# Kernel tuning notes

Measured on AMD Instinct MI355X. Metric: run time of the kernel, lower is better.

## Reference

```python
import jax, jax.numpy as jnp
import numpy as np

B, S, H, T = 32, 1024, 1024, 256
WINDOW = 2
ITERATIONS = 3


def setup_inputs() -> dict:
    key = jax.random.key(0)
    k1, k2, k3, k4, k5, k6 = jax.random.split(key, 6)
    token_feats = jax.random.normal(k1, (B, S, H), dtype=jnp.float32)
    unary_score = jax.random.normal(k2, (B, S, T), dtype=jnp.float32)
    lengths = jax.random.randint(k3, (B,), S // 2, S + 1)  # in [S/2, S]
    mask = (jnp.arange(S)[None, :] < lengths[:, None]).astype(jnp.float32)
    transitions = jax.random.normal(k4, (WINDOW, T, T), dtype=jnp.float32)
    start_transitions = jax.random.normal(k5, (WINDOW, T), dtype=jnp.float32)
    end_transitions = jax.random.normal(k6, (WINDOW, T), dtype=jnp.float32)
    return {
        "token_feats": token_feats,
        "unary_score": unary_score,
        "mask": mask,
        "transitions": transitions,
        "start_transitions": start_transitions,
        "end_transitions": end_transitions,
        "lengths": lengths,
    }


def reference(token_feats, unary_score, mask, transitions, start_transitions,
              end_transitions, lengths):
    # mask unary (and token_feats, as in original; token_feats is unused in
    # the plain-transitions second-order path)
    unary = unary_score * mask[..., None]        # [B,S,T]
    _ = token_feats * mask[..., None]
    q = unary
    batch_range = jnp.arange(q.shape[0])
    for _it in range(ITERATIONS):
        q = jax.nn.softmax(q, axis=-1)
        left_sum = jnp.zeros_like(q)
        right_sum = jnp.zeros_like(q)
        for j in range(1, WINDOW + 1):
            # message from left neighbor at distance j
            left_sum = left_sum.at[:, j:].add(
                jnp.einsum('nsa,ab->nsb', q[:, :-j], transitions[j - 1]))
            # message from right neighbor at distance j
            right_sum = right_sum.at[:, :-j].add(
                jnp.einsum('nsb,ab->nsa', q[:, j:], transitions[j - 1]))
            # end transitions scatter-add at position lengths - j
            right_sum = right_sum.at[batch_range, lengths - j].add(
                end_transitions[j - 1])
        msg = left_sum + right_sum
        # start transitions on first WINDOW positions (broadcast over batch)
        msg = msg.at[:, 0:WINDOW].add(start_transitions)
        q = unary + msg
        q = q * mask[..., None]
    return q
```

## Files before the change

### kernel.cpp

```cpp
#include <hip/hip_runtime.h>
#include <hip/hip_bf16.h>
#include <cstdint>


typedef __attribute__((ext_vector_type(4))) float f32x4;
typedef __attribute__((ext_vector_type(8))) short bf16x8;

__device__ __forceinline__ void load_lds16(const void* g, void* l) {
    __builtin_amdgcn_global_load_lds(
        (const __attribute__((address_space(1))) void*)g,
        (__attribute__((address_space(3))) void*)l, 16, 0, 0);
}

__global__ __launch_bounds__(256) void prep_wct(
    const float* __restrict__ trans,
    __hip_bfloat16* __restrict__ Pa, __hip_bfloat16* __restrict__ Pb,
    __hip_bfloat16* __restrict__ WcTt)
{
    int idx = blockIdx.x * 256 + threadIdx.x;
    if (idx < 32768) {
        int p = idx >> 10, sl = idx & 1023;
        int n = sl >> 2, cs = sl & 3;
        int gk = p * 4 + (cs ^ ((n >> 1) & 3));
        union { bf16x8 v; __hip_bfloat16 h[8]; } o;
        #pragma unroll
        for (int e = 0; e < 8; ++e) {
            int k = gk * 8 + e;
            int r = k >> 8, kk = k & 255;
            float v;
            if (r == 0)      v = trans[kk * 256 + n];
            else if (r == 1) v = trans[65536 + kk * 256 + n];
            else if (r == 2) v = trans[n * 256 + kk];
            else             v = trans[65536 + n * 256 + kk];
            o.h[e] = __float2bfloat16(v);
        }
        ((bf16x8*)WcTt)[idx] = o.v;
    } else if (idx < 40960) {
        int g = idx - 32768;
        __hip_bfloat16* P = (g & 4096) ? Pb : Pa;
        int rem = g & 4095;
        int b = rem >> 7, wr = (rem >> 5) & 3, ch = rem & 31;
        int row = b * 1028 + ((wr < 2) ? wr : 1024 + wr);
        bf16x8 z = {};
        *(bf16x8*)(P + row * 256 + ch * 8) = z;
    }
}

__global__ __launch_bounds__(512, 4) void mfvi_iter_k(
    const __hip_bfloat16* __restrict__ Pin,
    const __hip_bfloat16* __restrict__ WcTt,
    const float* __restrict__ unary, const int* __restrict__ lengths,
    const float* __restrict__ startT, const float* __restrict__ endT,
    __hip_bfloat16* __restrict__ Pout, float* __restrict__ out,
    int first_it, int final_it)
{
    __shared__ __hip_bfloat16 Ps[68 * 256];
    __shared__ __hip_bfloat16 Bs[2 * 256 * 32];
    __shared__ float redA[256];
    __shared__ float redB[256];

    int tid = threadIdx.x;
    int lane = tid & 63, w = tid >> 6;
    int cn = lane & 15, quad = lane >> 4;
    int wm = (w >> 2) * 32, wn = (w & 3) * 64;
    int nslice = w & 3;
    int tile = blockIdx.x;
    int b = tile >> 4, s0 = (tile & 15) << 6;
    int len = lengths[b];

    if (first_it) {
        for (int q = 0; q < 9; ++q) {
            int r = w + q * 8;
            if (r >= 68) break;
            int s = s0 + r - 2;
            int ch = lane >> 1;
            int slot = (ch & ~7) | ((ch ^ r) & 7);
            char* dst = (char*)Ps + r * 512 + slot * 16 + (lane & 1) * 8;
            if (s >= 0 && s < 1024) {
                float mval = (s < len) ? 1.f : 0.f;
                float4 x = *((const float4*)(unary + ((size_t)((b << 10) + s)) * 256 + lane * 4));
                x.x *= mval; x.y *= mval; x.z *= mval; x.w *= mval;
                float mx = fmaxf(fmaxf(x.x, x.y), fmaxf(x.z, x.w));
                #pragma unroll
                for (int o = 32; o; o >>= 1) mx = fmaxf(mx, __shfl_xor(mx, o));
                float ea = __expf(x.x - mx), eb = __expf(x.y - mx);
                float ec = __expf(x.z - mx), ed = __expf(x.w - mx);
                float sum = ea + eb + ec + ed;
                #pragma unroll
                for (int o = 32; o; o >>= 1) sum += __shfl_xor(sum, o);
                float inv = 1.0f / sum;
                union { ushort4 u; __hip_bfloat16 h[4]; } o4;
                o4.h[0] = __float2bfloat16(ea * inv);
                o4.h[1] = __float2bfloat16(eb * inv);
                o4.h[2] = __float2bfloat16(ec * inv);
                o4.h[3] = __float2bfloat16(ed * inv);
                *((ushort4*)dst) = o4.u;
            } else {
                ushort4 z = {0, 0, 0, 0};
                *((ushort4*)dst) = z;
            }
        }
    } else {
        const char* Pbase = (const char*)(Pin + ((size_t)b * 1028 + s0) * 256);
        #pragma unroll
        for (int t = 0; t < 5; ++t) {
            int c = t * 512 + tid;
            if (t < 4 || tid < 128) {
                int row = c >> 5, ch = c & 31;
                int gch = (ch & ~7) | ((ch ^ row) & 7);
                load_lds16(Pbase + row * 512 + gch * 16, (char*)Ps + c * 16);
            }
        }
    }
    __syncthreads();

    auto stageB = [&](int bb, int p) {
        #pragma unroll
        for (int c = 0; c < 2; ++c) {
            int sl = c * 512 + tid;
            load_lds16((const char*)WcTt + p * 16384 + sl * 16,
                       (char*)Bs + bb * 16384 + sl * 16);
        }
    };

    stageB(0, 0);
    stageB(1, 1);

    f32x4 acc[2][4] = {};

#define K_STEP(P, VMC, DOSTAGE) do {                                         \
    asm volatile("s_waitcnt vmcnt(" #VMC ")" ::: "memory");                  \
    __builtin_amdgcn_s_barrier();                                            \
    int region = (P) >> 3;                                                   \
    int delta = (region == 0) ? -1 : (region == 1) ? -2                      \
              : (region == 2) ?  1 : 2;                                      \
    int gcb = ((P) & 7) * 4 + quad;                                          \
    bf16x8 af[2], bfv[4];                                                    \
    _Pragma("unroll")                                                        \
    for (int i = 0; i < 2; ++i) {                                            \
        int r = wm + (i << 4) + cn + delta + 2;                              \
        int slot = (gcb & ~7) | ((gcb ^ r) & 7);                             \
        af[i] = *(const bf16x8*)((const char*)Ps + r * 512 + slot * 16);     \
    }                                                                        \
    _Pragma("unroll")                                                        \
    for (int j = 0; j < 4; ++j) {                                            \
        int n = wn + (j << 4) + cn;                                          \
        int cs = quad ^ ((n >> 1) & 3);                                      \
        bfv[j] = *(const bf16x8*)((const char*)Bs + ((P) & 1) * 16384        \
                                  + n * 64 + cs * 16);                       \
    }                                                                        \
    asm volatile("s_waitcnt lgkmcnt(0)" ::: "memory");                       \
    __builtin_amdgcn_s_barrier();                                            \
    if (DOSTAGE) stageB(((P) & 1), (P) + 2);                                 \
    __builtin_amdgcn_s_setprio(1);                                           \
    _Pragma("unroll")                                                        \
    for (int i = 0; i < 2; ++i)                                              \
        _Pragma("unroll")                                                    \
        for (int j = 0; j < 4; ++j)                                          \
            acc[i][j] = __builtin_amdgcn_mfma_f32_16x16x32_bf16(             \
                af[i], bfv[j], acc[i][j], 0, 0, 0);                          \
    __builtin_amdgcn_s_setprio(0);                                           \
} while (0)

    #pragma unroll
    for (int p = 0; p < 30; ++p) K_STEP(p, 2, true);
    K_STEP(30, 2, false);
    K_STEP(31, 0, false);
#undef K_STEP

    #pragma unroll
    for (int i = 0; i < 2; ++i)
        #pragma unroll
        for (int j = 0; j < 4; ++j) {
            int n = wn + (j << 4) + cn;
            #pragma unroll
            for (int r = 0; r < 4; ++r) {
                int s = s0 + wm + (i << 4) + (quad << 2) + r;
                float x = acc[i][j][r];
                if (s == 0)       x += startT[n];
                if (s == 1)       x += startT[256 + n];
                if (s == len - 1) x += endT[n];
                if (s == len - 2) x += endT[256 + n];
                long idx = ((long)((b << 10) + s)) * 256 + n;
                x += unary[idx];
                acc[i][j][r] = (s < len) ? x : 0.f;
            }
        }

    if (final_it) {
        #pragma unroll
        for (int i = 0; i < 2; ++i)
            #pragma unroll
            for (int j = 0; j < 4; ++j) {
                int n = wn + (j << 4) + cn;
                #pragma unroll
                for (int r = 0; r < 4; ++r) {
                    int s = s0 + wm + (i << 4) + (quad << 2) + r;
                    out[((long)((b << 10) + s)) * 256 + n] = acc[i][j][r];
                }
            }
        return;
    }

    #pragma unroll
    for (int i = 0; i < 2; ++i)
        #pragma unroll
        for (int r = 0; r < 4; ++r) {
            float m4 = fmaxf(fmaxf(acc[i][0][r], acc[i][1][r]),
                             fmaxf(acc[i][2][r], acc[i][3][r]));
            m4 = fmaxf(m4, __shfl_xor(m4, 1));
            m4 = fmaxf(m4, __shfl_xor(m4, 2));
            m4 = fmaxf(m4, __shfl_xor(m4, 4));
            m4 = fmaxf(m4, __shfl_xor(m4, 8));
            if (cn == 0)
                redA[(nslice << 6) + wm + (i << 4) + (quad << 2) + r] = m4;
        }
    __syncthreads();
    float M[2][4];
    #pragma unroll
    for (int i = 0; i < 2; ++i)
        #pragma unroll
        for (int r = 0; r < 4; ++r) {
            int row = wm + (i << 4) + (quad << 2) + r;
            M[i][r] = fmaxf(fmaxf(redA[row], redA[64 + row]),
                            fmaxf(redA[128 + row], redA[192 + row]));
        }
    #pragma unroll
    for (int i = 0; i < 2; ++i)
        #pragma unroll
        for (int r = 0; r < 4; ++r) {
            float s4 = 0.f;
            #pragma unroll
            for (int j = 0; j < 4; ++j) {
                float e = __expf(acc[i][j][r] - M[i][r]);
                acc[i][j][r] = e;
                s4 += e;
            }
            s4 += __shfl_xor(s4, 1);
            s4 += __shfl_xor(s4, 2);
            s4 += __shfl_xor(s4, 4);
            s4 += __shfl_xor(s4, 8);
            if (cn == 0)
                redB[(nslice << 6) + wm + (i << 4) + (quad << 2) + r] = s4;
        }
    __syncthreads();
    #pragma unroll
    for (int i = 0; i < 2; ++i)
        #pragma unroll
        for (int r = 0; r < 4; ++r) {
            int row = wm + (i << 4) + (quad << 2) + r;
            float inv = 1.0f / (redB[row] + redB[64 + row] +
                                redB[128 + row] + redB[192 + row]);
            int s = s0 + row;
            #pragma unroll
            for (int j = 0; j < 4; ++j) {
                int n = wn + (j << 4) + cn;
                Pout[((size_t)b * 1028 + 2 + s) * 256 + n] =
                    __float2bfloat16(acc[i][j][r] * inv);
            }
        }
}

extern "C" void kernel_launch(void* const* d_in, const int* in_sizes, int n_in,
                              void* d_out, int out_size, void* d_ws, size_t ws_size,
                              hipStream_t stream) {
    const float* unary  = (const float*)d_in[1];
    const float* trans  = (const float*)d_in[3];
    const float* startT = (const float*)d_in[4];
    const float* endT   = (const float*)d_in[5];
    const int*   lens   = (const int*)d_in[6];

    char* ws = (char*)d_ws;
    __hip_bfloat16* Pa   = (__hip_bfloat16*)ws;
    __hip_bfloat16* Pb   = (__hip_bfloat16*)(ws + ((size_t)32 << 20));
    __hip_bfloat16* WcTt = (__hip_bfloat16*)(ws + ((size_t)64 << 20));
    float* out = (float*)d_out;

    prep_wct<<<dim3(160), dim3(256), 0, stream>>>(trans, Pa, Pb, WcTt);
    mfvi_iter_k<<<dim3(512), dim3(512), 0, stream>>>(Pa, WcTt, unary, lens, startT, endT, Pb, nullptr, 1, 0);
    mfvi_iter_k<<<dim3(512), dim3(512), 0, stream>>>(Pb, WcTt, unary, lens, startT, endT, Pa, nullptr, 0, 0);
    mfvi_iter_k<<<dim3(512), dim3(512), 0, stream>>>(Pa, WcTt, unary, lens, startT, endT, nullptr, out, 0, 1);
}
```

Baseline: 278.7 us.

## Fuse three MFVI iterations into one kernel with halo recomputation

Replaces the three per-iteration launches with a single kernel that keeps q in LDS across all iterations. Each 64-row tile loads an 84-row window so the neighbor messages can be recomputed locally, using redundant halo rows instead of global round-trips. This removes the intermediate bf16 P buffers, two launches and the global write/read of q between iterations. In exchange each block does extra MFMA work for the 16 halo rows, with four of the eight waves carrying a third row tile, which unbalances the waves and adds LDS and register use.

Result: slower. 618.9 us (+122.1%).

```diff
diff --git a/kernel.cpp b/kernel.cpp
--- a/kernel.cpp
+++ b/kernel.cpp
@@ -13,106 +13,79 @@
 }
 
 __global__ __launch_bounds__(256) void prep_wct(
-    const float* __restrict__ trans,
-    __hip_bfloat16* __restrict__ Pa, __hip_bfloat16* __restrict__ Pb,
-    __hip_bfloat16* __restrict__ WcTt)
+    const float* __restrict__ trans, __hip_bfloat16* __restrict__ WcTt)
 {
     int idx = blockIdx.x * 256 + threadIdx.x;
-    if (idx < 32768) {
-        int p = idx >> 10, sl = idx & 1023;
-        int n = sl >> 2, cs = sl & 3;
-        int gk = p * 4 + (cs ^ ((n >> 1) & 3));
-        union { bf16x8 v; __hip_bfloat16 h[8]; } o;
-        #pragma unroll
-        for (int e = 0; e < 8; ++e) {
-            int k = gk * 8 + e;
-            int r = k >> 8, kk = k & 255;
-            float v;
-            if (r == 0)      v = trans[kk * 256 + n];
-            else if (r == 1) v = trans[65536 + kk * 256 + n];
-            else if (r == 2) v = trans[n * 256 + kk];
-            else             v = trans[65536 + n * 256 + kk];
-            o.h[e] = __float2bfloat16(v);
-        }
-        ((bf16x8*)WcTt)[idx] = o.v;
-    } else if (idx < 40960) {
-        int g = idx - 32768;
-        __hip_bfloat16* P = (g & 4096) ? Pb : Pa;
-        int rem = g & 4095;
-        int b = rem >> 7, wr = (rem >> 5) & 3, ch = rem & 31;
-        int row = b * 1028 + ((wr < 2) ? wr : 1024 + wr);
-        bf16x8 z = {};
-        *(bf16x8*)(P + row * 256 + ch * 8) = z;
+    int p = idx >> 10, sl = idx & 1023;
+    int n = sl >> 2, cs = sl & 3;
+    int gk = p * 4 + (cs ^ ((n >> 1) & 3));
+    union { bf16x8 v; __hip_bfloat16 h[8]; } o;
+    #pragma unroll
+    for (int e = 0; e < 8; ++e) {
+        int k = gk * 8 + e;
+        int r = k >> 8, kk = k & 255;
+        float v;
+        if (r == 0)      v = trans[kk * 256 + n];
+        else if (r == 1) v = trans[65536 + kk * 256 + n];
+        else if (r == 2) v = trans[n * 256 + kk];
+        else             v = trans[65536 + n * 256 + kk];
+        o.h[e] = __float2bfloat16(v);
     }
-}
-
-__global__ __launch_bounds__(512, 4) void mfvi_iter_k(
-    const __hip_bfloat16* __restrict__ Pin,
+    ((bf16x8*)WcTt)[idx] = o.v;
+}
+
+__global__ __launch_bounds__(512, 4) void mfvi_fused3(
     const __hip_bfloat16* __restrict__ WcTt,
     const float* __restrict__ unary, const int* __restrict__ lengths,
     const float* __restrict__ startT, const float* __restrict__ endT,
-    __hip_bfloat16* __restrict__ Pout, float* __restrict__ out,
-    int first_it, int final_it)
+    float* __restrict__ out)
 {
-    __shared__ __hip_bfloat16 Ps[68 * 256];
+    __shared__ __hip_bfloat16 Ps[84 * 256];
     __shared__ __hip_bfloat16 Bs[2 * 256 * 32];
-    __shared__ float redA[256];
-    __shared__ float redB[256];
+    __shared__ float redA[320];
+    __shared__ float redB[320];
 
     int tid = threadIdx.x;
     int lane = tid & 63, w = tid >> 6;
     int cn = lane & 15, quad = lane >> 4;
-    int wm = (w >> 2) * 32, wn = (w & 3) * 64;
+    bool wlo = (w < 4);
+    int wm = wlo ? 0 : 48, wn = (w & 3) * 64;
     int nslice = w & 3;
     int tile = blockIdx.x;
     int b = tile >> 4, s0 = (tile & 15) << 6;
     int len = lengths[b];
 
-    if (first_it) {
-        for (int q = 0; q < 9; ++q) {
-            int r = w + q * 8;
-            if (r >= 68) break;
-            int s = s0 + r - 2;
-            int ch = lane >> 1;
-            int slot = (ch & ~7) | ((ch ^ r) & 7);
-            char* dst = (char*)Ps + r * 512 + slot * 16 + (lane & 1) * 8;
-            if (s >= 0 && s < 1024) {
-                float mval = (s < len) ? 1.f : 0.f;
-                float4 x = *((const float4*)(unary + ((size_t)((b << 10) + s)) * 256 + lane * 4));
-                x.x *= mval; x.y *= mval; x.z *= mval; x.w *= mval;
-                float mx = fmaxf(fmaxf(x.x, x.y), fmaxf(x.z, x.w));
-                #pragma unroll
-                for (int o = 32; o; o >>= 1) mx = fmaxf(mx, __shfl_xor(mx, o));
-                float ea = __expf(x.x - mx), eb = __expf(x.y - mx);
-                float ec = __expf(x.z - mx), ed = __expf(x.w - mx);
-                float sum = ea + eb + ec + ed;
-                #pragma unroll
-                for (int o = 32; o; o >>= 1) sum += __shfl_xor(sum, o);
-                float inv = 1.0f / sum;
-                union { ushort4 u; __hip_bfloat16 h[4]; } o4;
-                o4.h[0] = __float2bfloat16(ea * inv);
-                o4.h[1] = __float2bfloat16(eb * inv);
-                o4.h[2] = __float2bfloat16(ec * inv);
-                o4.h[3] = __float2bfloat16(ed * inv);
-                *((ushort4*)dst) = o4.u;
-            } else {
-                ushort4 z = {0, 0, 0, 0};
-                *((ushort4*)dst) = z;
-            }
-        }
-    } else {
-        const char* Pbase = (const char*)(Pin + ((size_t)b * 1028 + s0) * 256);
-        #pragma unroll
-        for (int t = 0; t < 5; ++t) {
-            int c = t * 512 + tid;
-            if (t < 4 || tid < 128) {
-                int row = c >> 5, ch = c & 31;
-                int gch = (ch & ~7) | ((ch ^ row) & 7);
-                load_lds16(Pbase + row * 512 + gch * 16, (char*)Ps + c * 16);
-            }
+    for (int q = 0; q < 11; ++q) {
+        int pr = w + q * 8;
+        if (pr >= 84) break;
+        int s = s0 + pr - 10;
+        int ch = lane >> 1;
+        int slot = (ch & ~7) | ((ch ^ pr) & 7);
+        char* dst = (char*)Ps + pr * 512 + slot * 16 + (lane & 1) * 8;
+        if (s >= 0 && s < 1024) {
+            float mval = (s < len) ? 1.f : 0.f;
+            float4 x = *((const float4*)(unary + ((size_t)((b << 10) + s)) * 256 + lane * 4));
+            x.x *= mval; x.y *= mval; x.z *= mval; x.w *= mval;
+            float mx = fmaxf(fmaxf(x.x, x.y), fmaxf(x.z, x.w));
+            #pragma unroll
+            for (int o = 32; o; o >>= 1) mx = fmaxf(mx, __shfl_xor(mx, o));
+            float ea = __expf(x.x - mx), eb = __expf(x.y - mx);
+            float ec = __expf(x.z - mx), ed = __expf(x.w - mx);
+            float sum = ea + eb + ec + ed;
+            #pragma unroll
+            for (int o = 32; o; o >>= 1) sum += __shfl_xor(sum, o);
+            float inv = 1.0f / sum;
+            union { ushort4 u; __hip_bfloat16 h[4]; } o4;
+            o4.h[0] = __float2bfloat16(ea * inv);
+            o4.h[1] = __float2bfloat16(eb * inv);
+            o4.h[2] = __float2bfloat16(ec * inv);
+            o4.h[3] = __float2bfloat16(ed * inv);
+            *((ushort4*)dst) = o4.u;
+        } else {
+            ushort4 z = {0, 0, 0, 0};
+            *((ushort4*)dst) = z;
         }
     }
-    __syncthreads();
 
     auto stageB = [&](int bb, int p) {
         #pragma unroll
@@ -123,10 +96,13 @@
         }
     };
 
-    stageB(0, 0);
-    stageB(1, 1);
-
-    f32x4 acc[2][4] = {};
+    #pragma unroll 1
+    for (int it = 0; it < 3; ++it) {
+        __syncthreads();
+        stageB(0, 0);
+        stageB(1, 1);
+
+        f32x4 acc[3][4] = {};
 
 #define K_STEP(P, VMC, DOSTAGE) do {                                         \
     asm volatile("s_waitcnt vmcnt(" #VMC ")" ::: "memory");                  \
@@ -135,12 +111,17 @@
     int delta = (region == 0) ? -1 : (region == 1) ? -2                      \
               : (region == 2) ?  1 : 2;                                      \
     int gcb = ((P) & 7) * 4 + quad;                                          \
-    bf16x8 af[2], bfv[4];                                                    \
+    bf16x8 af[3], bfv[4];                                                    \
     _Pragma("unroll")                                                        \
     for (int i = 0; i < 2; ++i) {                                            \
         int r = wm + (i << 4) + cn + delta + 2;                              \
         int slot = (gcb & ~7) | ((gcb ^ r) & 7);                             \
         af[i] = *(const bf16x8*)((const char*)Ps + r * 512 + slot * 16);     \
+    }                                                                        \
+    if (wlo) {                                                               \
+        int r = 32 + cn + delta + 2;                                         \
+        int slot = (gcb & ~7) | ((gcb ^ r) & 7);                             \
+        af[2] = *(const bf16x8*)((const char*)Ps + r * 512 + slot * 16);     \
     }                                                                        \
     _Pragma("unroll")                                                        \
     for (int j = 0; j < 4; ++j) {                                            \
@@ -159,106 +140,132 @@
         for (int j = 0; j < 4; ++j)                                          \
             acc[i][j] = __builtin_amdgcn_mfma_f32_16x16x32_bf16(             \
                 af[i], bfv[j], acc[i][j], 0, 0, 0);                          \
+    if (wlo) {                                                               \
+        _Pragma("unroll")                                                    \
+        for (int j = 0; j < 4; ++j)                                          \
+            acc[2][j] = __builtin_amdgcn_mfma_f32_16x16x32_bf16(             \
+                af[2], bfv[j], acc[2][j], 0, 0, 0);                          \
+    }                                                                        \
     __builtin_amdgcn_s_setprio(0);                                           \
 } while (0)
 
-    #pragma unroll
-    for (int p = 0; p < 30; ++p) K_STEP(p, 2, true);
-    K_STEP(30, 2, false);
-    K_STEP(31, 0, false);
+        #pragma unroll
+        for (int p = 0; p < 30; ++p) K_STEP(p, 2, true);
+        K_STEP(30, 2, false);
+        K_STEP(31, 0, false);
 #undef K_STEP
 
-    #pragma unroll
-    for (int i = 0; i < 2; ++i)
-        #pragma unroll
-        for (int j = 0; j < 4; ++j) {
-            int n = wn + (j << 4) + cn;
-            #pragma unroll
-            for (int r = 0; r < 4; ++r) {
-                int s = s0 + wm + (i << 4) + (quad << 2) + r;
-                float x = acc[i][j][r];
-                if (s == 0)       x += startT[n];
-                if (s == 1)       x += startT[256 + n];
-                if (s == len - 1) x += endT[n];
-                if (s == len - 2) x += endT[256 + n];
-                long idx = ((long)((b << 10) + s)) * 256 + n;
-                x += unary[idx];
-                acc[i][j][r] = (s < len) ? x : 0.f;
-            }
-        }
-
-    if (final_it) {
-        #pragma unroll
-        for (int i = 0; i < 2; ++i)
+        #pragma unroll
+        for (int i = 0; i < 3; ++i) {
+            if (i == 2 && !wlo) continue;
             #pragma unroll
             for (int j = 0; j < 4; ++j) {
                 int n = wn + (j << 4) + cn;
                 #pragma unroll
                 for (int r = 0; r < 4; ++r) {
-                    int s = s0 + wm + (i << 4) + (quad << 2) + r;
-                    out[((long)((b << 10) + s)) * 256 + n] = acc[i][j][r];
-                }
-            }
-        return;
+                    int lr = wm + (i << 4) + (quad << 2) + r;
+                    int s = s0 + lr - 8;
+                    float x = acc[i][j][r];
+                    if (s == 0)       x += startT[n];
+                    if (s == 1)       x += startT[256 + n];
+                    if (s == len - 1) x += endT[n];
+                    if (s == len - 2) x += endT[256 + n];
+                    if (s >= 0 && s < 1024)
+                        x += unary[((long)((b << 10) + s)) * 256 + n];
+                    acc[i][j][r] = (s >= 0 && s < len) ? x : 0.f;
+                }
+            }
+        }
+
+        if (it == 2) {
+            #pragma unroll
+            for (int i = 0; i < 3; ++i) {
+                if (i == 2 && !wlo) continue;
+                #pragma unroll
+                for (int j = 0; j < 4; ++j) {
+                    int n = wn + (j << 4) + cn;
+                    #pragma unroll
+                    for (int r = 0; r < 4; ++r) {
+                        int lr = wm + (i << 4) + (quad << 2) + r;
+                        if (lr < 8 || lr >= 72) continue;
+                        int s = s0 + lr - 8;
+                        out[((long)((b << 10) + s)) * 256 + n] = acc[i][j][r];
+                    }
+                }
+            }
+            return;
+        }
+
+        #pragma unroll
+        for (int i = 0; i < 3; ++i) {
+            if (i == 2 && !wlo) continue;
+            #pragma unroll
+            for (int r = 0; r < 4; ++r) {
+                float m4 = fmaxf(fmaxf(acc[i][0][r], acc[i][1][r]),
+                                 fmaxf(acc[i][2][r], acc[i][3][r]));
+                m4 = fmaxf(m4, __shfl_xor(m4, 1));
+                m4 = fmaxf(m4, __shfl_xor(m4, 2));
+                m4 = fmaxf(m4, __shfl_xor(m4, 4));
+                m4 = fmaxf(m4, __shfl_xor(m4, 8));
+                if (cn == 0)
+                    redA[nslice * 80 + wm + (i << 4) + (quad << 2) + r] = m4;
+            }
+        }
+        __syncthreads();
+        float M[3][4];
+        #pragma unroll
+        for (int i = 0; i < 3; ++i) {
+            if (i == 2 && !wlo) continue;
+            #pragma unroll
+            for (int r = 0; r < 4; ++r) {
+                int lr = wm + (i << 4) + (quad << 2) + r;
+                M[i][r] = fmaxf(fmaxf(redA[lr], redA[80 + lr]),
+                                fmaxf(redA[160 + lr], redA[240 + lr]));
+            }
+        }
+        #pragma unroll
+        for (int i = 0; i < 3; ++i) {
+            if (i == 2 && !wlo) continue;
+            #pragma unroll
+            for (int r = 0; r < 4; ++r) {
+                float s4 = 0.f;
+                #pragma unroll
+                for (int j = 0; j < 4; ++j) {
+                    float e = __expf(acc[i][j][r] - M[i][r]);
+                    acc[i][j][r] = e;
+                    s4 += e;
+                }
+                s4 += __shfl_xor(s4, 1);
+                s4 += __shfl_xor(s4, 2);
+                s4 += __shfl_xor(s4, 4);
+                s4 += __shfl_xor(s4, 8);
+                if (cn == 0)
+                    redB[nslice * 80 + wm + (i << 4) + (quad << 2) + r] = s4;
+            }
+        }
+        __syncthreads();
+        #pragma unroll
+        for (int i = 0; i < 3; ++i) {
+            if (i == 2 && !wlo) continue;
+            #pragma unroll
+            for (int r = 0; r < 4; ++r) {
+                int lr = wm + (i << 4) + (quad << 2) + r;
+                int s = s0 + lr - 8;
+                bool inr = (s >= 0 && s < 1024);
+                float inv = 1.0f / (redB[lr] + redB[80 + lr] +
+                                    redB[160 + lr] + redB[240 + lr]);
+                int pr = lr + 2;
+                #pragma unroll
+                for (int j = 0; j < 4; ++j) {
+                    int n = wn + (j << 4) + cn;
+                    int ch = n >> 3;
+                    int slot = (ch & ~7) | ((ch ^ pr) & 7);
+                    *((__hip_bfloat16*)((char*)Ps + pr * 512 + slot * 16 + (n & 7) * 2)) =
+                        __float2bfloat16(inr ? acc[i][j][r] * inv : 0.f);
+                }
+            }
+        }
     }
-
-    #pragma unroll
-    for (int i = 0; i < 2; ++i)
-        #pragma unroll
-        for (int r = 0; r < 4; ++r) {
-            float m4 = fmaxf(fmaxf(acc[i][0][r], acc[i][1][r]),
-                             fmaxf(acc[i][2][r], acc[i][3][r]));
-            m4 = fmaxf(m4, __shfl_xor(m4, 1));
-            m4 = fmaxf(m4, __shfl_xor(m4, 2));
-            m4 = fmaxf(m4, __shfl_xor(m4, 4));
-            m4 = fmaxf(m4, __shfl_xor(m4, 8));
-            if (cn == 0)
-                redA[(nslice << 6) + wm + (i << 4) + (quad << 2) + r] = m4;
-        }
-    __syncthreads();
-    float M[2][4];
-    #pragma unroll
-    for (int i = 0; i < 2; ++i)
-        #pragma unroll
-        for (int r = 0; r < 4; ++r) {
-            int row = wm + (i << 4) + (quad << 2) + r;
-            M[i][r] = fmaxf(fmaxf(redA[row], redA[64 + row]),
-                            fmaxf(redA[128 + row], redA[192 + row]));
-        }
-    #pragma unroll
-    for (int i = 0; i < 2; ++i)
-        #pragma unroll
-        for (int r = 0; r < 4; ++r) {
-            float s4 = 0.f;
-            #pragma unroll
-            for (int j = 0; j < 4; ++j) {
-                float e = __expf(acc[i][j][r] - M[i][r]);
-                acc[i][j][r] = e;
-                s4 += e;
-            }
-            s4 += __shfl_xor(s4, 1);
-            s4 += __shfl_xor(s4, 2);
-            s4 += __shfl_xor(s4, 4);
-            s4 += __shfl_xor(s4, 8);
-            if (cn == 0)
-                redB[(nslice << 6) + wm + (i << 4) + (quad << 2) + r] = s4;
-        }
-    __syncthreads();
-    #pragma unroll
-    for (int i = 0; i < 2; ++i)
-        #pragma unroll
-        for (int r = 0; r < 4; ++r) {
-            int row = wm + (i << 4) + (quad << 2) + r;
-            float inv = 1.0f / (redB[row] + redB[64 + row] +
-                                redB[128 + row] + redB[192 + row]);
-            int s = s0 + row;
-            #pragma unroll
-            for (int j = 0; j < 4; ++j) {
-                int n = wn + (j << 4) + cn;
-                Pout[((size_t)b * 1028 + 2 + s) * 256 + n] =
-                    __float2bfloat16(acc[i][j][r] * inv);
-            }
-        }
 }
 
 extern "C" void kernel_launch(void* const* d_in, const int* in_sizes, int n_in,
@@ -270,14 +277,9 @@
     const float* endT   = (const float*)d_in[5];
     const int*   lens   = (const int*)d_in[6];
 
-    char* ws = (char*)d_ws;
-    __hip_bfloat16* Pa   = (__hip_bfloat16*)ws;
-    __hip_bfloat16* Pb   = (__hip_bfloat16*)(ws + ((size_t)32 << 20));
-    __hip_bfloat16* WcTt = (__hip_bfloat16*)(ws + ((size_t)64 << 20));
+    __hip_bfloat16* WcTt = (__hip_bfloat16*)d_ws;
     float* out = (float*)d_out;
 
-    prep_wct<<<dim3(160), dim3(256), 0, stream>>>(trans, Pa, Pb, WcTt);
-    mfvi_iter_k<<<dim3(512), dim3(512), 0, stream>>>(Pa, WcTt, unary, lens, startT, endT, Pb, nullptr, 1, 0);
-    mfvi_iter_k<<<dim3(512), dim3(512), 0, stream>>>(Pb, WcTt, unary, lens, startT, endT, Pa, nullptr, 0, 0);
-    mfvi_iter_k<<<dim3(512), dim3(512), 0, stream>>>(Pa, WcTt, unary, lens, startT, endT, nullptr, out, 0, 1);
-}
+    prep_wct<<<dim3(128), dim3(256), 0, stream>>>(trans, WcTt);
+    mfvi_fused3<<<dim3(512), dim3(512), 0, stream>>>(WcTt, unary, lens, startT, endT, out);
+}
```
